# Performance work log

Hardware: AMD Instinct MI355X
Metric: run time of the kernel (lower is better)

Reference implementation:

```python
import jax, jax.numpy as jnp
import numpy as np

BATCH, LENGTH, DIM = 8, 65536, 128
MAX_N_PEAKS = 512


def setup_inputs() -> dict:
    rng = np.random.default_rng(0)
    # per-sample number of peaks (each sample also has one trailing dropped chunk)
    n_peaks = rng.integers(400, MAX_N_PEAKS + 1, size=BATCH)
    chunk_sizes = []
    for i in range(BATCH):
        # n_peaks[i] cut points -> n_peaks[i]+1 chunks summing exactly to LENGTH
        cuts = np.sort(rng.choice(np.arange(1, LENGTH), size=int(n_peaks[i]), replace=False))
        sizes = np.diff(np.concatenate([[0], cuts, [LENGTH]]))
        chunk_sizes.append(sizes)
    chunk_size = np.concatenate(chunk_sizes).astype(np.int32)
    key = jax.random.key(0)
    x = jax.random.normal(key, (BATCH, LENGTH, DIM), dtype=jnp.float32)
    return {
        "x": x,
        "chunk_size": jnp.asarray(chunk_size),
        "n_peaks": jnp.asarray(n_peaks, dtype=jnp.int32),
        "max_n_peaks": MAX_N_PEAKS,
    }


def reference(x, chunk_size, n_peaks, max_n_peaks):
    # x: (B, L, D); chunk_size: (total_chunks,) summing to B*L;
    # n_peaks: (B,); sample i owns chunks [pool_start[i], pool_start[i]+n_peaks[i]+1),
    # the last chunk of each sample is dropped (matches pool_end = pool_idx - 1).
    batch, length, dim = x.shape
    total_chunks = chunk_size.shape[0]  # static
    x_flat = x.reshape(-1, dim)  # (B*L, D)

    # one fused segment-mean over all chunks
    seg_ids = jnp.repeat(jnp.arange(total_chunks), chunk_size,
                         total_repeat_length=batch * length)
    sums = jax.ops.segment_sum(x_flat, seg_ids, num_segments=total_chunks)
    counts = jnp.maximum(chunk_size, 1).astype(x.dtype)  # empty chunk -> zeros
    means = sums / counts[:, None]  # (total_chunks, D)

    # map chunk -> (sample, peak slot), scatter into padded output
    chunks_per_sample = n_peaks + 1
    pool_start = jnp.concatenate(
        [jnp.zeros((1,), n_peaks.dtype), jnp.cumsum(chunks_per_sample)[:-1]])
    sample_of_chunk = jnp.repeat(jnp.arange(batch), chunks_per_sample,
                                 total_repeat_length=total_chunks)
    peak_pos = jnp.arange(total_chunks) - pool_start[sample_of_chunk]
    valid = peak_pos < n_peaks[sample_of_chunk]  # drops trailing chunk per sample
    dest = jnp.where(valid, peak_pos, max_n_peaks)  # invalid -> scratch row
    out = jnp.zeros((batch, max_n_peaks + 1, dim), x.dtype)
    out = out.at[sample_of_chunk, dest].set(means)
    return out[:, :max_n_peaks]  # (B, max_n_peaks, D), zero-padded
```

## Files before the change

kernel.cpp:

```cpp
#include <hip/hip_runtime.h>
#include <hip/hip_bf16.h>


#define SCAN_THREADS 256
#define NSPLIT 4

__global__ __launch_bounds__(SCAN_THREADS) void scan_kernel(
    const int* __restrict__ chunk_size, const int* __restrict__ n_peaks,
    int total_chunks, int batch,
    int* __restrict__ chunk_start, int* __restrict__ pool_start) {
  __shared__ int partials[SCAN_THREADS];
  const int t = threadIdx.x;
  const int items = (total_chunks + SCAN_THREADS - 1) / SCAN_THREADS;
  const int begin = t * items;
  const int end = min(begin + items, total_chunks);

  int local = 0;
  for (int i = begin; i < end; ++i) local += chunk_size[i];
  partials[t] = local;
  __syncthreads();

  for (int off = 1; off < SCAN_THREADS; off <<= 1) {
    int v = (t >= off) ? partials[t - off] : 0;
    __syncthreads();
    partials[t] += v;
    __syncthreads();
  }

  int run = (t == 0) ? 0 : partials[t - 1];
  for (int i = begin; i < end; ++i) {
    chunk_start[i] = run;
    run += chunk_size[i];
  }

  if (t == 0) {
    int acc = 0;
    for (int i = 0; i < batch; ++i) {
      pool_start[i] = acc;
      acc += n_peaks[i] + 1;
    }
  }
}

__global__ __launch_bounds__(256) void split_sum_kernel(
    const float* __restrict__ x, const int* __restrict__ chunk_size,
    const int* __restrict__ chunk_start, float4* __restrict__ split_sums) {
  const int c = blockIdx.x >> 2;
  const int s = blockIdx.x & 3;
  const int t = threadIdx.x;
  const int dim4 = t & 31;
  const int r0 = t >> 5;

  const int start = chunk_start[c];
  const int size = chunk_size[c];
  const int rps = (size + NSPLIT - 1) >> 2;
  const int r_begin = s * rps;
  const int r_end = min(r_begin + rps, size);

  const float4* __restrict__ xp = (const float4*)x + (size_t)start * 32;
  float4 acc = make_float4(0.f, 0.f, 0.f, 0.f);
#pragma unroll 4
  for (int r = r_begin + r0; r < r_end; r += 8) {
    float4 v = xp[(size_t)r * 32 + dim4];
    acc.x += v.x; acc.y += v.y; acc.z += v.z; acc.w += v.w;
  }

  __shared__ float4 red[256];
  red[t] = acc;
  __syncthreads();

  if (t < 32) {
    float4 sum = red[t];
#pragma unroll
    for (int k = 1; k < 8; ++k) {
      float4 v = red[t + 32 * k];
      sum.x += v.x; sum.y += v.y; sum.z += v.z; sum.w += v.w;
    }
    split_sums[((size_t)blockIdx.x) * 32 + t] = sum;
  }
}

__global__ __launch_bounds__(256) void combine_kernel(
    const float4* __restrict__ split_sums, const int* __restrict__ chunk_size,
    const int* __restrict__ n_peaks, const int* __restrict__ pool_start,
    float4* __restrict__ out, int max_n_peaks, int n_slots) {
  const int t = threadIdx.x;
  const int slot = blockIdx.x * 8 + (t >> 5);
  const int dim4 = t & 31;
  if (slot >= n_slots) return;
  const int i = slot / max_n_peaks;
  const int p = slot % max_n_peaks;

  float4 m = make_float4(0.f, 0.f, 0.f, 0.f);
  if (p < n_peaks[i]) {
    const int c = pool_start[i] + p;
    float4 sum = make_float4(0.f, 0.f, 0.f, 0.f);
#pragma unroll
    for (int k = 0; k < NSPLIT; ++k) {
      float4 v = split_sums[((size_t)c * NSPLIT + k) * 32 + dim4];
      sum.x += v.x; sum.y += v.y; sum.z += v.z; sum.w += v.w;
    }
    const int sz = chunk_size[c];
    const float inv = 1.0f / (float)(sz > 0 ? sz : 1);
    m = make_float4(sum.x * inv, sum.y * inv, sum.z * inv, sum.w * inv);
  }
  out[(size_t)slot * 32 + dim4] = m;
}

extern "C" void kernel_launch(void* const* d_in, const int* in_sizes, int n_in,
                              void* d_out, int out_size, void* d_ws, size_t ws_size,
                              hipStream_t stream) {
  const float* x = (const float*)d_in[0];
  const int* chunk_size = (const int*)d_in[1];
  const int* n_peaks = (const int*)d_in[2];
  const int total_chunks = in_sizes[1];
  const int batch = in_sizes[2];
  const int dim = 128;
  const int max_n_peaks = out_size / (batch * dim);
  float* out = (float*)d_out;

  int* chunk_start = (int*)d_ws;
  int* pool_start = chunk_start + total_chunks;
  size_t off = ((size_t)(total_chunks + batch) * sizeof(int) + 15) & ~(size_t)15;
  float4* split_sums = (float4*)((char*)d_ws + off);

  scan_kernel<<<1, SCAN_THREADS, 0, stream>>>(chunk_size, n_peaks, total_chunks,
                                              batch, chunk_start, pool_start);

  split_sum_kernel<<<total_chunks * NSPLIT, 256, 0, stream>>>(
      x, chunk_size, chunk_start, split_sums);

  const int n_slots = batch * max_n_peaks;
  combine_kernel<<<(n_slots + 7) / 8, 256, 0, stream>>>(
      split_sums, chunk_size, n_peaks, pool_start, (float4*)out, max_n_peaks,
      n_slots);
}
```

Before: 369.7 us.

## Replace per-chunk split reduction with fixed row tiles and atomic accumulation

The segment sum now uses fixed 128-row tiles instead of one block per chunk quarter. Each tile binary-searches the chunk that contains its first row, walks the chunk boundaries inside the tile, and atomically adds each partial sum into a zeroed per-chunk accumulator. This is meant to remove load imbalance from very uneven chunk sizes and the overhead of many tiny blocks. The zeroing is folded into a multi-block scan kernel, and the combine step now reads a single sum per chunk. The cost is float atomics, with nondeterministic summation order, and an extra block barrier for every segment inside a tile.

Measured after the change: 374.2 us. Within noise of the previous version (+1.2%).

```diff
diff --git a/kernel.cpp b/kernel.cpp
--- a/kernel.cpp
+++ b/kernel.cpp
@@ -3,12 +3,21 @@
 
 
 #define SCAN_THREADS 256
-#define NSPLIT 4
+#define TILE_ROWS 128
 
-__global__ __launch_bounds__(SCAN_THREADS) void scan_kernel(
+#define SCAN_BLOCKS 64
+__global__ __launch_bounds__(SCAN_THREADS) void scan_zero_kernel(
     const int* __restrict__ chunk_size, const int* __restrict__ n_peaks,
     int total_chunks, int batch,
-    int* __restrict__ chunk_start, int* __restrict__ pool_start) {
+    int* __restrict__ chunk_start, int* __restrict__ pool_start,
+    float4* __restrict__ sums) {
+  const int nf4 = total_chunks * 32;
+  for (int idx = blockIdx.x * SCAN_THREADS + threadIdx.x; idx < nf4;
+       idx += SCAN_BLOCKS * SCAN_THREADS) {
+    sums[idx] = make_float4(0.f, 0.f, 0.f, 0.f);
+  }
+  if (blockIdx.x != 0) return;
+
   __shared__ int partials[SCAN_THREADS];
   const int t = threadIdx.x;
   const int items = (total_chunks + SCAN_THREADS - 1) / SCAN_THREADS;
@@ -42,46 +51,60 @@
   }
 }
 
-__global__ __launch_bounds__(256) void split_sum_kernel(
-    const float* __restrict__ x, const int* __restrict__ chunk_size,
-    const int* __restrict__ chunk_start, float4* __restrict__ split_sums) {
-  const int c = blockIdx.x >> 2;
-  const int s = blockIdx.x & 3;
+__global__ __launch_bounds__(256) void tile_sum_kernel(
+    const float* __restrict__ x, const int* __restrict__ chunk_start,
+    float* __restrict__ sums, int total_chunks, int total_rows) {
   const int t = threadIdx.x;
   const int dim4 = t & 31;
   const int r0 = t >> 5;
+  const int tile_begin = blockIdx.x * TILE_ROWS;
+  const int tile_end = min(tile_begin + TILE_ROWS, total_rows);
 
-  const int start = chunk_start[c];
-  const int size = chunk_size[c];
-  const int rps = (size + NSPLIT - 1) >> 2;
-  const int r_begin = s * rps;
-  const int r_end = min(r_begin + rps, size);
+  int lo = 0, hi = total_chunks - 1;
+  while (lo < hi) {
+    int mid = (lo + hi + 1) >> 1;
+    if (chunk_start[mid] <= tile_begin) lo = mid; else hi = mid - 1;
+  }
+  int c = lo;
 
-  const float4* __restrict__ xp = (const float4*)x + (size_t)start * 32;
-  float4 acc = make_float4(0.f, 0.f, 0.f, 0.f);
+  const float4* __restrict__ xp = (const float4*)x;
+  __shared__ float4 red[256];
+
+  int seg_begin = tile_begin;
+  while (seg_begin < tile_end) {
+    const int chunk_end = (c + 1 < total_chunks) ? chunk_start[c + 1] : total_rows;
+    const int seg_end = min(chunk_end, tile_end);
+
+    float4 acc = make_float4(0.f, 0.f, 0.f, 0.f);
 #pragma unroll 4
-  for (int r = r_begin + r0; r < r_end; r += 8) {
-    float4 v = xp[(size_t)r * 32 + dim4];
-    acc.x += v.x; acc.y += v.y; acc.z += v.z; acc.w += v.w;
-  }
+    for (int r = seg_begin + r0; r < seg_end; r += 8) {
+      float4 v = xp[(size_t)r * 32 + dim4];
+      acc.x += v.x; acc.y += v.y; acc.z += v.z; acc.w += v.w;
+    }
 
-  __shared__ float4 red[256];
-  red[t] = acc;
-  __syncthreads();
-
-  if (t < 32) {
-    float4 sum = red[t];
+    red[t] = acc;
+    __syncthreads();
+    if (t < 32) {
+      float4 s = red[t];
 #pragma unroll
-    for (int k = 1; k < 8; ++k) {
-      float4 v = red[t + 32 * k];
-      sum.x += v.x; sum.y += v.y; sum.z += v.z; sum.w += v.w;
+      for (int k = 1; k < 8; ++k) {
+        float4 v = red[t + 32 * k];
+        s.x += v.x; s.y += v.y; s.z += v.z; s.w += v.w;
+      }
+      float* dst = sums + (size_t)c * 128 + t * 4;
+      atomicAdd(dst + 0, s.x);
+      atomicAdd(dst + 1, s.y);
+      atomicAdd(dst + 2, s.z);
+      atomicAdd(dst + 3, s.w);
     }
-    split_sums[((size_t)blockIdx.x) * 32 + t] = sum;
+    __syncthreads();
+    seg_begin = seg_end;
+    ++c;
   }
 }
 
 __global__ __launch_bounds__(256) void combine_kernel(
-    const float4* __restrict__ split_sums, const int* __restrict__ chunk_size,
+    const float4* __restrict__ sums, const int* __restrict__ chunk_size,
     const int* __restrict__ n_peaks, const int* __restrict__ pool_start,
     float4* __restrict__ out, int max_n_peaks, int n_slots) {
   const int t = threadIdx.x;
@@ -94,15 +117,10 @@
   float4 m = make_float4(0.f, 0.f, 0.f, 0.f);
   if (p < n_peaks[i]) {
     const int c = pool_start[i] + p;
-    float4 sum = make_float4(0.f, 0.f, 0.f, 0.f);
-#pragma unroll
-    for (int k = 0; k < NSPLIT; ++k) {
-      float4 v = split_sums[((size_t)c * NSPLIT + k) * 32 + dim4];
-      sum.x += v.x; sum.y += v.y; sum.z += v.z; sum.w += v.w;
-    }
+    float4 s = sums[(size_t)c * 32 + dim4];
     const int sz = chunk_size[c];
     const float inv = 1.0f / (float)(sz > 0 ? sz : 1);
-    m = make_float4(sum.x * inv, sum.y * inv, sum.z * inv, sum.w * inv);
+    m = make_float4(s.x * inv, s.y * inv, s.z * inv, s.w * inv);
   }
   out[(size_t)slot * 32 + dim4] = m;
 }
@@ -117,21 +135,24 @@
   const int batch = in_sizes[2];
   const int dim = 128;
   const int max_n_peaks = out_size / (batch * dim);
+  const int total_rows = in_sizes[0] / dim;
   float* out = (float*)d_out;
 
   int* chunk_start = (int*)d_ws;
   int* pool_start = chunk_start + total_chunks;
   size_t off = ((size_t)(total_chunks + batch) * sizeof(int) + 15) & ~(size_t)15;
-  float4* split_sums = (float4*)((char*)d_ws + off);
+  float* sums = (float*)((char*)d_ws + off);
 
-  scan_kernel<<<1, SCAN_THREADS, 0, stream>>>(chunk_size, n_peaks, total_chunks,
-                                              batch, chunk_start, pool_start);
+  scan_zero_kernel<<<SCAN_BLOCKS, SCAN_THREADS, 0, stream>>>(
+      chunk_size, n_peaks, total_chunks, batch, chunk_start, pool_start,
+      (float4*)sums);
 
-  split_sum_kernel<<<total_chunks * NSPLIT, 256, 0, stream>>>(
-      x, chunk_size, chunk_start, split_sums);
+  const int n_tiles = (total_rows + TILE_ROWS - 1) / TILE_ROWS;
+  tile_sum_kernel<<<n_tiles, 256, 0, stream>>>(x, chunk_start, sums,
+                                               total_chunks, total_rows);
 
   const int n_slots = batch * max_n_peaks;
   combine_kernel<<<(n_slots + 7) / 8, 256, 0, stream>>>(
-      split_sums, chunk_size, n_peaks, pool_start, (float4*)out, max_n_peaks,
-      n_slots);
+      (const float4*)sums, chunk_size, n_peaks, pool_start, (float4*)out,
+      max_n_peaks, n_slots);
 }
```
